# Optimization experiments

Hardware: AMD Instinct MI355X
Metric: run time of the kernel (lower is better)

Reference implementation:

```python
import jax, jax.numpy as jnp
import numpy as np

N = 100000   # nodes
E = 1600000  # directed edges
HID = 64


def gat_conv(x, src, dst, W, a_src, a_dst, b, heads, out_ch):
    """PyG-style GATConv (add_self_loops=True, negative_slope=0.2, concat)."""
    n = x.shape[0]
    h = (x @ W).reshape(n, heads, out_ch)              # [N,H,C]
    loop = jnp.arange(n, dtype=src.dtype)
    s = jnp.concatenate([src, loop])                   # self loops appended
    d = jnp.concatenate([dst, loop])
    alpha_src = jnp.sum(h * a_src, axis=-1)            # [N,H]
    alpha_dst = jnp.sum(h * a_dst, axis=-1)            # [N,H]
    alpha = jax.nn.leaky_relu(alpha_src[s] + alpha_dst[d], 0.2)  # [E+N,H]
    # segment softmax over incoming edges of each destination node
    amax = jax.ops.segment_max(alpha, d, num_segments=n)
    alpha = jnp.exp(alpha - amax[d])
    asum = jax.ops.segment_sum(alpha, d, num_segments=n)
    alpha = alpha / (asum[d] + 1e-16)
    msg = h[s] * alpha[:, :, None]                     # [E+N,H,C]
    out = jax.ops.segment_sum(msg, d, num_segments=n)  # [N,H,C]
    return out.reshape(n, heads * out_ch) + b


def setup_inputs() -> dict:
    key = jax.random.key(0)
    ks = jax.random.split(key, 22)
    rn = lambda k, shp, s=0.1: (jax.random.normal(k, shp, jnp.float32) * s)
    inp = {
        "x": jax.random.normal(ks[0], (N, 2), jnp.float32),
        "edge_index": jax.random.randint(ks[1], (2, E), 0, N, dtype=jnp.int32),
        "edge_attr": jax.random.normal(ks[2], (E, 2), jnp.float32),
        # node encoder
        "enc_W": rn(ks[3], (2, HID)), "enc_b": rn(ks[4], (HID,)),
        # gat1: heads=4, out=16
        "g1_W": rn(ks[5], (HID, HID)), "g1_as": rn(ks[6], (4, 16)),
        "g1_ad": rn(ks[7], (4, 16)), "g1_b": rn(ks[8], (HID,)),
        # gat2: heads=1, out=64
        "g2_W": rn(ks[9], (HID, HID)), "g2_as": rn(ks[10], (1, HID)),
        "g2_ad": rn(ks[11], (1, HID)), "g2_b": rn(ks[12], (HID,)),
        # node head
        "no_W1": rn(ks[13], (HID, HID)), "no_b1": rn(ks[14], (HID,)),
        "no_W2": rn(ks[15], (HID, 2)), "no_b2": rn(ks[16], (2,)),
        # edge head: in = 2*HID + 2 = 130
        "eo_W1": rn(ks[17], (2 * HID + 2, HID)), "eo_b1": rn(ks[18], (HID,)),
        "eo_W2": rn(ks[19], (HID, 1)), "eo_b2": rn(ks[20], (1,)),
    }
    return inp


def reference(x, edge_index, edge_attr, enc_W, enc_b,
              g1_W, g1_as, g1_ad, g1_b,
              g2_W, g2_as, g2_ad, g2_b,
              no_W1, no_b1, no_W2, no_b2,
              eo_W1, eo_b1, eo_W2, eo_b2):
    src, dst = edge_index[0], edge_index[1]
    h = x @ enc_W + enc_b                                    # node encoder (dropout = eval identity)
    h = jax.nn.elu(gat_conv(h, src, dst, g1_W, g1_as, g1_ad, g1_b, 4, 16))
    h = gat_conv(h, src, dst, g2_W, g2_as, g2_ad, g2_b, 1, HID)
    e_in = jnp.concatenate([h[src], h[dst], edge_attr], axis=-1)  # [E,130]
    node_pred = jnp.tanh(jax.nn.leaky_relu(h @ no_W1 + no_b1, 0.01) @ no_W2 + no_b2)
    edge_pred = jnp.tanh(jax.nn.leaky_relu(e_in @ eo_W1 + eo_b1, 0.01) @ eo_W2 + eo_b2)[:, 0]
    return edge_pred, node_pred
```

## Files before the change

### kernel.cpp

```cpp
#include <hip/hip_runtime.h>
#include <hip/hip_fp16.h>
#include <math.h>


typedef _Float16 half8_t __attribute__((ext_vector_type(8)));
typedef float floatx4 __attribute__((ext_vector_type(4)));

__global__ void k_scatter(const int* __restrict__ src, const int* __restrict__ dst,
                          int E, int NB, int cap, int* cursor,
                          unsigned int* __restrict__ ebuf,
                          const float* __restrict__ encW, const float* __restrict__ encb,
                          const float* __restrict__ g1W, float* __restrict__ Mc){
  __shared__ int hist[256];
  __shared__ int base[256];
  int t = threadIdx.x;
  if (blockIdx.x == 0 && t < 64){
    float m0 = 0.f, m1 = 0.f, cc = 0.f;
    for (int k = 0; k < 64; ++k){
      float g = g1W[k * 64 + t];
      m0 = fmaf(encW[k], g, m0);
      m1 = fmaf(encW[64 + k], g, m1);
      cc = fmaf(encb[k], g, cc);
    }
    Mc[t] = m0; Mc[64 + t] = m1; Mc[128 + t] = cc;
  }
  hist[t] = 0;
  __syncthreads();
  int cbase = blockIdx.x * 2048;
  int sv[8], bk[8], dl[8];
  #pragma unroll
  for (int i = 0; i < 8; ++i){
    int e = cbase + i * 256 + t;
    if (e < E){
      int d = dst[e];
      sv[i] = src[e]; bk[i] = d >> 9; dl[i] = d & 511;
      atomicAdd(&hist[bk[i]], 1);
    } else bk[i] = -1;
  }
  __syncthreads();
  int c = hist[t];
  base[t] = (t < NB && c > 0) ? (t * cap + atomicAdd(&cursor[t], c)) : 0;
  __syncthreads();
  hist[t] = 0;
  __syncthreads();
  #pragma unroll
  for (int i = 0; i < 8; ++i){
    if (bk[i] >= 0){
      int r = atomicAdd(&hist[bk[i]], 1);
      int p = base[bk[i]] + r;
      if (p < (bk[i] + 1) * cap)
        ebuf[p] = (unsigned)sv[i] | ((unsigned)dl[i] << 17);
    }
  }
}

__global__ void k_bucket_build(const int* __restrict__ cursor, int cap, int N,
                               unsigned int* ebuf, int* __restrict__ rstart,
                               int* __restrict__ rend){
  __shared__ unsigned int ent[12288];
  __shared__ int cnts[512];
  __shared__ int aux[512];
  int b = blockIdx.x, t = threadIdx.x;
  int base = b * cap;
  int cnt = cursor[b];
  if (cnt > cap) cnt = cap;
  for (int i = t; i < cnt; i += 512) ent[i] = ebuf[base + i];
  cnts[t] = 0;
  __syncthreads();
  for (int i = t; i < cnt; i += 512) atomicAdd(&cnts[ent[i] >> 17], 1);
  __syncthreads();
  int v = cnts[t];
  aux[t] = v;
  __syncthreads();
  for (int off = 1; off < 512; off <<= 1){
    int x = (t >= off) ? aux[t - off] : 0;
    __syncthreads();
    aux[t] += x;
    __syncthreads();
  }
  int incl = aux[t];
  int node = (b << 9) + t;
  if (node < N){ rstart[node] = base + incl - v; rend[node] = base + incl; }
  cnts[t] = incl - v;
  __syncthreads();
  for (int i = t; i < cnt; i += 512){
    unsigned int en = ent[i];
    int pos = atomicAdd(&cnts[en >> 17], 1);
    ebuf[base + pos] = en;
  }
}

template<int H>
__global__ void k_palpha(const int* __restrict__ cursor, int cap,
                         const unsigned int* __restrict__ ebuf,
                         const float* __restrict__ as, const float* __restrict__ ad,
                         float* __restrict__ palpha){
  int blk = blockIdx.x;
  int b = blk >> 2, part = blk & 3;
  int base = b * cap;
  int cnt = cursor[b];
  if (cnt > cap) cnt = cap;
  for (int i = part * 256 + threadIdx.x; i < cnt; i += 1024){
    unsigned int en = ebuf[base + i];
    int s = en & 0x1FFFFu;
    int d = (b << 9) + (en >> 17);
    if (H == 4){
      float4 sv = ((const float4*)as)[s];
      float4 dv = ((const float4*)ad)[d];
      float a0 = sv.x + dv.x, a1 = sv.y + dv.y, a2 = sv.z + dv.z, a3 = sv.w + dv.w;
      a0 = a0 > 0.f ? a0 : 0.2f * a0;
      a1 = a1 > 0.f ? a1 : 0.2f * a1;
      a2 = a2 > 0.f ? a2 : 0.2f * a2;
      a3 = a3 > 0.f ? a3 : 0.2f * a3;
      float4 pv = {__expf(a0), __expf(a1), __expf(a2), __expf(a3)};
      ((float4*)palpha)[base + i] = pv;
    } else {
      float a = as[s] + ad[d];
      a = a > 0.f ? a : 0.2f * a;
      palpha[base + i] = __expf(a);
    }
  }
}

__global__ void k_fuse1(const float* __restrict__ x, const float* __restrict__ Mc,
                        const float* __restrict__ a_s, const float* __restrict__ a_d,
                        __half* __restrict__ hw, float* __restrict__ alpha_s,
                        float* __restrict__ alpha_d, int n){
  int idx = blockIdx.x * blockDim.x + threadIdx.x;
  if (idx >= n * 64) return;
  int node = idx >> 6, j = idx & 63;
  float acc = fmaf(x[node * 2 + 0], Mc[j], fmaf(x[node * 2 + 1], Mc[64 + j], Mc[128 + j]));
  hw[idx] = __float2half(acc);
  float ps = acc * a_s[j];
  float pd = acc * a_d[j];
  #pragma unroll
  for (int off = 1; off < 16; off <<= 1){
    ps += __shfl_xor(ps, off);
    pd += __shfl_xor(pd, off);
  }
  if ((j & 15) == 0){
    int h = j >> 4;
    alpha_s[node * 4 + h] = ps;
    alpha_d[node * 4 + h] = pd;
  }
}

__global__ __launch_bounds__(256) void k_hw_mfma(
    const float* __restrict__ hin, const float* __restrict__ W,
    const float* __restrict__ a_s, const float* __restrict__ a_d,
    __half* __restrict__ hw, float* __restrict__ alpha_s,
    float* __restrict__ alpha_d, int n){
  __shared__ float redS[4][16];
  __shared__ float redD[4][16];
  int t = threadIdx.x;
  int lane = t & 63, wave = t >> 6;
  int l15 = lane & 15, quad = lane >> 4;
  int ch = wave * 16 + l15;
  half8_t b0, b1;
  #pragma unroll
  for (int j = 0; j < 8; ++j){
    b0[j] = (_Float16)W[(quad * 8 + j) * 64 + ch];
    b1[j] = (_Float16)W[(quad * 8 + j + 32) * 64 + ch];
  }
  float asv = a_s[ch], adv = a_d[ch];
  int base = blockIdx.x * 64;
  for (int it = 0; it < 4; ++it){
    int tb = base + it * 16;
    if (tb >= n) break;
    int arn = tb + l15; if (arn >= n) arn = n - 1;
    const float* arow = hin + (size_t)arn * 64 + quad * 8;
    half8_t a0, a1;
    #pragma unroll
    for (int j = 0; j < 8; ++j){
      a0[j] = (_Float16)arow[j];
      a1[j] = (_Float16)arow[j + 32];
    }
    floatx4 acc = {0.f, 0.f, 0.f, 0.f};
    acc = __builtin_amdgcn_mfma_f32_16x16x32_f16(a0, b0, acc, 0, 0, 0);
    acc = __builtin_amdgcn_mfma_f32_16x16x32_f16(a1, b1, acc, 0, 0, 0);
    float ps[4], pd[4];
    #pragma unroll
    for (int r = 0; r < 4; ++r){
      int node = tb + quad * 4 + r;
      if (node < n) hw[(size_t)node * 64 + ch] = __float2half(acc[r]);
      ps[r] = acc[r] * asv;
      pd[r] = acc[r] * adv;
      #pragma unroll
      for (int off = 1; off < 16; off <<= 1){
        ps[r] += __shfl_xor(ps[r], off);
        pd[r] += __shfl_xor(pd[r], off);
      }
    }
    if (l15 == 0){
      #pragma unroll
      for (int r = 0; r < 4; ++r){
        redS[wave][quad * 4 + r] = ps[r];
        redD[wave][quad * 4 + r] = pd[r];
      }
    }
    __syncthreads();
    if (t < 16 && tb + t < n){
      alpha_s[tb + t] = redS[0][t] + redS[1][t] + redS[2][t] + redS[3][t];
      alpha_d[tb + t] = redD[0][t] + redD[1][t] + redD[2][t] + redD[3][t];
    }
    __syncthreads();
  }
}

template<int H, bool ELU_ACT>
__global__ void k_agg(const __half* __restrict__ hw, const float* __restrict__ palpha,
                      const float* __restrict__ alpha_s, const float* __restrict__ alpha_d,
                      const int* __restrict__ rstart, const int* __restrict__ rend,
                      const unsigned int* __restrict__ ebuf,
                      const float* __restrict__ bias, float* __restrict__ hout, int n){
  int node = (blockIdx.x * blockDim.x + threadIdx.x) >> 6;
  int lane = threadIdx.x & 63;
  int g = lane >> 3, jj = lane & 7;
  if (node >= n) return;
  int hidx = (jj * H) >> 3;
  int start = rstart[node], end = rend[node];
  float acc[8] = {0.f,0.f,0.f,0.f,0.f,0.f,0.f,0.f};
  float psum = 0.f;
  if (g == 0){
    float a = alpha_s[node * H + hidx] + alpha_d[node * H + hidx];
    a = a > 0.f ? a : 0.2f * a;
    float p = __expf(a);
    psum = p;
    float4 rv = *(const float4*)(hw + (size_t)node * 64 + jj * 8);
    const __half2* hp = (const __half2*)&rv;
    #pragma unroll
    for (int k = 0; k < 4; ++k){
      float2 f = __half22float2(hp[k]);
      acc[2 * k] = p * f.x; acc[2 * k + 1] = p * f.y;
    }
  }
  int i = start + g;
  for (; i + 8 < end; i += 16){
    unsigned int e0 = ebuf[i], e1 = ebuf[i + 8];
    int s0 = e0 & 0x1FFFF, s1 = e1 & 0x1FFFF;
    float p0 = palpha[(size_t)i * H + hidx];
    float p1 = palpha[(size_t)(i + 8) * H + hidx];
    float4 r0 = *(const float4*)(hw + (size_t)s0 * 64 + jj * 8);
    float4 r1 = *(const float4*)(hw + (size_t)s1 * 64 + jj * 8);
    const __half2* h0 = (const __half2*)&r0;
    const __half2* h1 = (const __half2*)&r1;
    psum += p0 + p1;
    #pragma unroll
    for (int k = 0; k < 4; ++k){
      float2 f0 = __half22float2(h0[k]);
      float2 f1 = __half22float2(h1[k]);
      acc[2 * k]     = fmaf(p0, f0.x, fmaf(p1, f1.x, acc[2 * k]));
      acc[2 * k + 1] = fmaf(p0, f0.y, fmaf(p1, f1.y, acc[2 * k + 1]));
    }
  }
  if (i < end){
    unsigned int en = ebuf[i];
    int s = en & 0x1FFFF;
    float p = palpha[(size_t)i * H + hidx];
    float4 rv = *(const float4*)(hw + (size_t)s * 64 + jj * 8);
    const __half2* hp = (const __half2*)&rv;
    psum += p;
    #pragma unroll
    for (int k = 0; k < 4; ++k){
      float2 f = __half22float2(hp[k]);
      acc[2 * k]     = fmaf(p, f.x, acc[2 * k]);
      acc[2 * k + 1] = fmaf(p, f.y, acc[2 * k + 1]);
    }
  }
  #pragma unroll
  for (int off = 8; off < 64; off <<= 1){
    psum += __shfl_xor(psum, off);
    #pragma unroll
    for (int k = 0; k < 8; ++k) acc[k] += __shfl_xor(acc[k], off);
  }
  if (g == 0){
    float inv = 1.f / (psum + 1e-16f);
    float4 bv0 = ((const float4*)bias)[2 * jj];
    float4 bv1 = ((const float4*)bias)[2 * jj + 1];
    float o[8];
    o[0] = fmaf(acc[0], inv, bv0.x); o[1] = fmaf(acc[1], inv, bv0.y);
    o[2] = fmaf(acc[2], inv, bv0.z); o[3] = fmaf(acc[3], inv, bv0.w);
    o[4] = fmaf(acc[4], inv, bv1.x); o[5] = fmaf(acc[5], inv, bv1.y);
    o[6] = fmaf(acc[6], inv, bv1.z); o[7] = fmaf(acc[7], inv, bv1.w);
    if (ELU_ACT){
      #pragma unroll
      for (int k = 0; k < 8; ++k) o[k] = o[k] > 0.f ? o[k] : (__expf(o[k]) - 1.f);
    }
    float4 ov0 = {o[0], o[1], o[2], o[3]};
    float4 ov1 = {o[4], o[5], o[6], o[7]};
    float* dstp = hout + (size_t)node * 64 + jj * 8;
    *(float4*)dstp = ov0;
    *(float4*)(dstp + 4) = ov1;
  }
}

__global__ __launch_bounds__(256) void k_heads_mfma(
    const float* __restrict__ h, const float* __restrict__ eoW1,
    const float* __restrict__ noW1, const float* __restrict__ nob1,
    const float* __restrict__ noW2, const float* __restrict__ nob2,
    __half* __restrict__ P1, __half* __restrict__ P2,
    float* __restrict__ outN, int n){
  __shared__ float redP[4][16][2];
  int t = threadIdx.x;
  int lane = t & 63, wave = t >> 6;
  int l15 = lane & 15, quad = lane >> 4;
  int ch = wave * 16 + l15;
  half8_t bP1a, bP1b, bP2a, bP2b, bNa, bNb;
  #pragma unroll
  for (int j = 0; j < 8; ++j){
    int k0 = quad * 8 + j, k1 = k0 + 32;
    bP1a[j] = (_Float16)eoW1[k0 * 64 + ch];
    bP1b[j] = (_Float16)eoW1[k1 * 64 + ch];
    bP2a[j] = (_Float16)eoW1[(k0 + 64) * 64 + ch];
    bP2b[j] = (_Float16)eoW1[(k1 + 64) * 64 + ch];
    bNa[j]  = (_Float16)noW1[k0 * 64 + ch];
    bNb[j]  = (_Float16)noW1[k1 * 64 + ch];
  }
  float b1v = nob1[ch];
  float w20 = noW2[ch * 2 + 0], w21 = noW2[ch * 2 + 1];
  float b20 = nob2[0], b21 = nob2[1];
  int base = blockIdx.x * 64;
  for (int it = 0; it < 4; ++it){
    int tb = base + it * 16;
    if (tb >= n) break;
    int arn = tb + l15; if (arn >= n) arn = n - 1;
    const float* arow = h + (size_t)arn * 64 + quad * 8;
    half8_t a0, a1;
    #pragma unroll
    for (int j = 0; j < 8; ++j){
      a0[j] = (_Float16)arow[j];
      a1[j] = (_Float16)arow[j + 32];
    }
    floatx4 ac1 = {0.f,0.f,0.f,0.f}, ac2 = {0.f,0.f,0.f,0.f}, acN = {0.f,0.f,0.f,0.f};
    ac1 = __builtin_amdgcn_mfma_f32_16x16x32_f16(a0, bP1a, ac1, 0, 0, 0);
    ac1 = __builtin_amdgcn_mfma_f32_16x16x32_f16(a1, bP1b, ac1, 0, 0, 0);
    ac2 = __builtin_amdgcn_mfma_f32_16x16x32_f16(a0, bP2a, ac2, 0, 0, 0);
    ac2 = __builtin_amdgcn_mfma_f32_16x16x32_f16(a1, bP2b, ac2, 0, 0, 0);
    acN = __builtin_amdgcn_mfma_f32_16x16x32_f16(a0, bNa, acN, 0, 0, 0);
    acN = __builtin_amdgcn_mfma_f32_16x16x32_f16(a1, bNb, acN, 0, 0, 0);
    float p0[4], p1[4];
    #pragma unroll
    for (int r = 0; r < 4; ++r){
      int node = tb + quad * 4 + r;
      if (node < n){
        P1[(size_t)node * 64 + ch] = __float2half(ac1[r]);
        P2[(size_t)node * 64 + ch] = __float2half(ac2[r]);
      }
      float v = acN[r] + b1v;
      v = v > 0.f ? v : 0.01f * v;
      p0[r] = v * w20;
      p1[r] = v * w21;
      #pragma unroll
      for (int off = 1; off < 16; off <<= 1){
        p0[r] += __shfl_xor(p0[r], off);
        p1[r] += __shfl_xor(p1[r], off);
      }
    }
    if (l15 == 0){
      #pragma unroll
      for (int r = 0; r < 4; ++r){
        redP[wave][quad * 4 + r][0] = p0[r];
        redP[wave][quad * 4 + r][1] = p1[r];
      }
    }
    __syncthreads();
    if (t < 16 && tb + t < n){
      float s0 = redP[0][t][0] + redP[1][t][0] + redP[2][t][0] + redP[3][t][0];
      float s1 = redP[0][t][1] + redP[1][t][1] + redP[2][t][1] + redP[3][t][1];
      outN[(size_t)(tb + t) * 2 + 0] = tanhf(s0 + b20);
      outN[(size_t)(tb + t) * 2 + 1] = tanhf(s1 + b21);
    }
    __syncthreads();
  }
}

__global__ void k_edge_head(const __half* __restrict__ P1h, const __half* __restrict__ P2h,
                            const int* __restrict__ src, const int* __restrict__ dst,
                            const float* __restrict__ eattr, const float* __restrict__ eoW1,
                            const float* __restrict__ b1, const float* __restrict__ W2,
                            const float* __restrict__ b2, float* __restrict__ out, int E){
  int lane = threadIdx.x & 63;
  int jj = lane & 7, q = lane >> 3;
  int wid = (blockIdx.x * blockDim.x + threadIdx.x) >> 6;
  int nw = (gridDim.x * blockDim.x) >> 6;

  const float4* rAq = (const float4*)(eoW1 + 8192);
  const float4* rBq = (const float4*)(eoW1 + 8256);
  const float4* b1q = (const float4*)b1;
  const float4* w2q = (const float4*)W2;
  float4 tA0 = rAq[2 * jj], tA1 = rAq[2 * jj + 1];
  float4 tB0 = rBq[2 * jj], tB1 = rBq[2 * jj + 1];
  float4 tb0 = b1q[2 * jj], tb1 = b1q[2 * jj + 1];
  float4 tw0 = w2q[2 * jj], tw1 = w2q[2 * jj + 1];
  float ra[8] = {tA0.x, tA0.y, tA0.z, tA0.w, tA1.x, tA1.y, tA1.z, tA1.w};
  float rb[8] = {tB0.x, tB0.y, tB0.z, tB0.w, tB1.x, tB1.y, tB1.z, tB1.w};
  float bb[8] = {tb0.x, tb0.y, tb0.z, tb0.w, tb1.x, tb1.y, tb1.z, tb1.w};
  float w2[8] = {tw0.x, tw0.y, tw0.z, tw0.w, tw1.x, tw1.y, tw1.z, tw1.w};
  float b2v = b2[0];

  const float4* P1q = (const float4*)P1h;
  const float4* P2q = (const float4*)P2h;
  const float2* eav = (const float2*)eattr;

  int groups = (E + 15) >> 4;
  for (int g = wid; g < groups; g += nw){
    int e0 = g * 16 + q, e1 = e0 + 8;
    bool act0 = (e0 < E), act1 = (e1 < E);
    float p0 = 0.f, p1 = 0.f;
    if (act0){
      int s = src[e0], d = dst[e0];
      float2 ea = eav[e0];
      float4 g1 = P1q[(size_t)s * 8 + jj];
      float4 g2 = P2q[(size_t)d * 8 + jj];
      const __half2* h1 = (const __half2*)&g1;
      const __half2* h2 = (const __half2*)&g2;
      #pragma unroll
      for (int k = 0; k < 4; ++k){
        float2 u = __half22float2(h1[k]);
        float2 w = __half22float2(h2[k]);
        float ta = u.x + w.x + bb[2 * k];
        float tb = u.y + w.y + bb[2 * k + 1];
        ta = fmaf(ea.x, ra[2 * k], fmaf(ea.y, rb[2 * k], ta));
        tb = fmaf(ea.x, ra[2 * k + 1], fmaf(ea.y, rb[2 * k + 1], tb));
        ta = ta > 0.f ? ta : 0.01f * ta;
        tb = tb > 0.f ? tb : 0.01f * tb;
        p0 = fmaf(ta, w2[2 * k], fmaf(tb, w2[2 * k + 1], p0));
      }
    }
    if (act1){
      int s = src[e1], d = dst[e1];
      float2 ea = eav[e1];
      float4 g1 = P1q[(size_t)s * 8 + jj];
      float4 g2 = P2q[(size_t)d * 8 + jj];
      const __half2* h1 = (const __half2*)&g1;
      const __half2* h2 = (const __half2*)&g2;
      #pragma unroll
      for (int k = 0; k < 4; ++k){
        float2 u = __half22float2(h1[k]);
        float2 w = __half22float2(h2[k]);
        float ta = u.x + w.x + bb[2 * k];
        float tb = u.y + w.y + bb[2 * k + 1];
        ta = fmaf(ea.x, ra[2 * k], fmaf(ea.y, rb[2 * k], ta));
        tb = fmaf(ea.x, ra[2 * k + 1], fmaf(ea.y, rb[2 * k + 1], tb));
        ta = ta > 0.f ? ta : 0.01f * ta;
        tb = tb > 0.f ? tb : 0.01f * tb;
        p1 = fmaf(ta, w2[2 * k], fmaf(tb, w2[2 * k + 1], p1));
      }
    }
    #pragma unroll
    for (int off = 1; off < 8; off <<= 1){
      p0 += __shfl_xor(p0, off);
      p1 += __shfl_xor(p1, off);
    }
    if (jj == 0){
      if (act0) out[e0] = tanhf(p0 + b2v);
      if (act1) out[e1] = tanhf(p1 + b2v);
    }
  }
}

extern "C" void kernel_launch(void* const* d_in, const int* in_sizes, int n_in,
                              void* d_out, int out_size, void* d_ws, size_t ws_size,
                              hipStream_t stream){
  const float* x    = (const float*)d_in[0];
  const int*   eidx = (const int*)  d_in[1];
  const float* ea   = (const float*)d_in[2];
  const float* encW = (const float*)d_in[3];
  const float* encb = (const float*)d_in[4];
  const float* g1W  = (const float*)d_in[5];
  const float* g1as = (const float*)d_in[6];
  const float* g1ad = (const float*)d_in[7];
  const float* g1b  = (const float*)d_in[8];
  const float* g2W  = (const float*)d_in[9];
  const float* g2as = (const float*)d_in[10];
  const float* g2ad = (const float*)d_in[11];
  const float* g2b  = (const float*)d_in[12];
  const float* noW1 = (const float*)d_in[13];
  const float* nob1 = (const float*)d_in[14];
  const float* noW2 = (const float*)d_in[15];
  const float* nob2 = (const float*)d_in[16];
  const float* eoW1 = (const float*)d_in[17];
  const float* eob1 = (const float*)d_in[18];
  const float* eoW2 = (const float*)d_in[19];
  const float* eob2 = (const float*)d_in[20];

  const int N = in_sizes[0] / 2;
  const int E = in_sizes[1] / 2;
  const int* src = eidx;
  const int* dst = eidx + E;

  const int NB = (N + 511) >> 9;
  int avg = (E + NB - 1) / NB;
  int cap = avg + avg / 4 + 64;
  if (cap > 12288) cap = 12288;

  char* ws = (char*)d_ws;
  size_t off = 0;
  auto alloc = [&](size_t bytes) -> void* {
    void* p = ws + off;
    off = (off + bytes + 255) & ~(size_t)255;
    return p;
  };
  float*  bufA  = (float*) alloc((size_t)N * 64 * 4);
  __half* bufH  = (__half*)alloc((size_t)N * 64 * 2);
  __half* P1h   = (__half*)alloc((size_t)N * 64 * 2);
  __half* P2h   = (__half*)alloc((size_t)N * 64 * 2);
  float*  as    = (float*) alloc((size_t)N * 4 * 4);
  float*  ad    = (float*) alloc((size_t)N * 4 * 4);
  int* rstart   = (int*)   alloc((size_t)N * 4);
  int* rend     = (int*)   alloc((size_t)N * 4);
  unsigned int* ebuf = (unsigned int*)alloc((size_t)NB * cap * 4);
  float* palphaB = (float*)alloc((size_t)NB * cap * 16);
  int* cursor   = (int*)   alloc((size_t)NB * 4);
  float* Mc     = (float*) alloc(192 * 4);

  hipMemsetAsync(cursor, 0, (size_t)NB * 4, stream);
  k_scatter<<<(E + 2047) / 2048, 256, 0, stream>>>(src, dst, E, NB, cap, cursor, ebuf,
                                                   encW, encb, g1W, Mc);
  k_fuse1<<<(N * 64 + 255) / 256, 256, 0, stream>>>(x, Mc, g1as, g1ad, bufH, as, ad, N);
  k_bucket_build<<<NB, 512, 0, stream>>>(cursor, cap, N, ebuf, rstart, rend);
  k_palpha<4><<<NB * 4, 256, 0, stream>>>(cursor, cap, ebuf, as, ad, palphaB);
  k_agg<4, true><<<(N + 3) / 4, 256, 0, stream>>>(bufH, palphaB, as, ad,
                                                  rstart, rend, ebuf, g1b, bufA, N);
  k_hw_mfma<<<(N + 63) / 64, 256, 0, stream>>>(bufA, g2W, g2as, g2ad, bufH, as, ad, N);
  k_palpha<1><<<NB * 4, 256, 0, stream>>>(cursor, cap, ebuf, as, ad, palphaB);
  k_agg<1, false><<<(N + 3) / 4, 256, 0, stream>>>(bufH, palphaB, as, ad,
                                                   rstart, rend, ebuf, g2b, bufA, N);
  float* out = (float*)d_out;
  k_heads_mfma<<<(N + 63) / 64, 256, 0, stream>>>(bufA, eoW1, noW1, nob1, noW2, nob2,
                                                  P1h, P2h, out + E, N);
  k_edge_head<<<2048, 256, 0, stream>>>(P1h, P2h, src, dst, ea,
                                        eoW1, eob1, eoW2, eob2, out, E);
}
```

Before: 384.5 us.

## Shrink destination buckets to 128 nodes and store intermediate features in fp16

Destination buckets for the CSR build go from 512 nodes to 128. That gives about 782 buckets with smaller shared-memory footprints, so k_bucket_build can run with more blocks, less LDS per block and 256 threads. The scatter kernel's histogram loops now iterate over NB, since NB exceeds the thread count. Separately, the aggregation output is stored as fp16 rather than fp32, and the downstream MFMA kernels read it with vector half8 loads, halving that traffic and dropping the per-element conversions. Risks: many more global cursor atomics in the scatter step, a small cap of 2700 that could overflow buckets, and lower intermediate precision.

```diff
diff --git a/kernel.cpp b/kernel.cpp
--- a/kernel.cpp
+++ b/kernel.cpp
@@ -11,8 +11,8 @@
                           unsigned int* __restrict__ ebuf,
                           const float* __restrict__ encW, const float* __restrict__ encb,
                           const float* __restrict__ g1W, float* __restrict__ Mc){
-  __shared__ int hist[256];
-  __shared__ int base[256];
+  __shared__ int hist[800];
+  __shared__ int base[800];
   int t = threadIdx.x;
   if (blockIdx.x == 0 && t < 64){
     float m0 = 0.f, m1 = 0.f, cc = 0.f;
@@ -24,7 +24,7 @@
     }
     Mc[t] = m0; Mc[64 + t] = m1; Mc[128 + t] = cc;
   }
-  hist[t] = 0;
+  for (int i = t; i < NB; i += 256) hist[i] = 0;
   __syncthreads();
   int cbase = blockIdx.x * 2048;
   int sv[8], bk[8], dl[8];
@@ -33,15 +33,16 @@
     int e = cbase + i * 256 + t;
     if (e < E){
       int d = dst[e];
-      sv[i] = src[e]; bk[i] = d >> 9; dl[i] = d & 511;
+      sv[i] = src[e]; bk[i] = d >> 7; dl[i] = d & 127;
       atomicAdd(&hist[bk[i]], 1);
     } else bk[i] = -1;
   }
   __syncthreads();
-  int c = hist[t];
-  base[t] = (t < NB && c > 0) ? (t * cap + atomicAdd(&cursor[t], c)) : 0;
-  __syncthreads();
-  hist[t] = 0;
+  for (int i = t; i < NB; i += 256){
+    int c = hist[i];
+    base[i] = (c > 0) ? (i * cap + atomicAdd(&cursor[i], c)) : 0;
+    hist[i] = 0;
+  }
   __syncthreads();
   #pragma unroll
   for (int i = 0; i < 8; ++i){
@@ -57,33 +58,36 @@
 __global__ void k_bucket_build(const int* __restrict__ cursor, int cap, int N,
                                unsigned int* ebuf, int* __restrict__ rstart,
                                int* __restrict__ rend){
-  __shared__ unsigned int ent[12288];
-  __shared__ int cnts[512];
-  __shared__ int aux[512];
+  __shared__ unsigned int ent[2700];
+  __shared__ int cnts[128];
+  __shared__ int aux[128];
   int b = blockIdx.x, t = threadIdx.x;
   int base = b * cap;
   int cnt = cursor[b];
   if (cnt > cap) cnt = cap;
-  for (int i = t; i < cnt; i += 512) ent[i] = ebuf[base + i];
-  cnts[t] = 0;
-  __syncthreads();
-  for (int i = t; i < cnt; i += 512) atomicAdd(&cnts[ent[i] >> 17], 1);
-  __syncthreads();
-  int v = cnts[t];
-  aux[t] = v;
-  __syncthreads();
-  for (int off = 1; off < 512; off <<= 1){
-    int x = (t >= off) ? aux[t - off] : 0;
+  for (int i = t; i < cnt; i += 256) ent[i] = ebuf[base + i];
+  if (t < 128) cnts[t] = 0;
+  __syncthreads();
+  for (int i = t; i < cnt; i += 256) atomicAdd(&cnts[ent[i] >> 17], 1);
+  __syncthreads();
+  int v = 0;
+  if (t < 128){ v = cnts[t]; aux[t] = v; }
+  __syncthreads();
+  for (int off = 1; off < 128; off <<= 1){
+    int x = 0;
+    if (t < 128 && t >= off) x = aux[t - off];
     __syncthreads();
-    aux[t] += x;
+    if (t < 128) aux[t] += x;
     __syncthreads();
   }
-  int incl = aux[t];
-  int node = (b << 9) + t;
-  if (node < N){ rstart[node] = base + incl - v; rend[node] = base + incl; }
-  cnts[t] = incl - v;
-  __syncthreads();
-  for (int i = t; i < cnt; i += 512){
+  if (t < 128){
+    int incl = aux[t];
+    int node = (b << 7) + t;
+    if (node < N){ rstart[node] = base + incl - v; rend[node] = base + incl; }
+    cnts[t] = incl - v;
+  }
+  __syncthreads();
+  for (int i = t; i < cnt; i += 256){
     unsigned int en = ent[i];
     int pos = atomicAdd(&cnts[en >> 17], 1);
     ebuf[base + pos] = en;
@@ -103,7 +107,7 @@
   for (int i = part * 256 + threadIdx.x; i < cnt; i += 1024){
     unsigned int en = ebuf[base + i];
     int s = en & 0x1FFFFu;
-    int d = (b << 9) + (en >> 17);
+    int d = (b << 7) + (en >> 17);
     if (H == 4){
       float4 sv = ((const float4*)as)[s];
       float4 dv = ((const float4*)ad)[d];
@@ -146,7 +150,7 @@
 }
 
 __global__ __launch_bounds__(256) void k_hw_mfma(
-    const float* __restrict__ hin, const float* __restrict__ W,
+    const __half* __restrict__ hin, const float* __restrict__ W,
     const float* __restrict__ a_s, const float* __restrict__ a_d,
     __half* __restrict__ hw, float* __restrict__ alpha_s,
     float* __restrict__ alpha_d, int n){
@@ -168,13 +172,9 @@
     int tb = base + it * 16;
     if (tb >= n) break;
     int arn = tb + l15; if (arn >= n) arn = n - 1;
-    const float* arow = hin + (size_t)arn * 64 + quad * 8;
-    half8_t a0, a1;
-    #pragma unroll
-    for (int j = 0; j < 8; ++j){
-      a0[j] = (_Float16)arow[j];
-      a1[j] = (_Float16)arow[j + 32];
-    }
+    const __half* arow = hin + (size_t)arn * 64 + quad * 8;
+    half8_t a0 = *(const half8_t*)arow;
+    half8_t a1 = *(const half8_t*)(arow + 32);
     floatx4 acc = {0.f, 0.f, 0.f, 0.f};
     acc = __builtin_amdgcn_mfma_f32_16x16x32_f16(a0, b0, acc, 0, 0, 0);
     acc = __builtin_amdgcn_mfma_f32_16x16x32_f16(a1, b1, acc, 0, 0, 0);
@@ -212,7 +212,7 @@
                       const float* __restrict__ alpha_s, const float* __restrict__ alpha_d,
                       const int* __restrict__ rstart, const int* __restrict__ rend,
                       const unsigned int* __restrict__ ebuf,
-                      const float* __restrict__ bias, float* __restrict__ hout, int n){
+                      const float* __restrict__ bias, __half* __restrict__ hout, int n){
   int node = (blockIdx.x * blockDim.x + threadIdx.x) >> 6;
   int lane = threadIdx.x & 63;
   int g = lane >> 3, jj = lane & 7;
@@ -286,16 +286,15 @@
       #pragma unroll
       for (int k = 0; k < 8; ++k) o[k] = o[k] > 0.f ? o[k] : (__expf(o[k]) - 1.f);
     }
-    float4 ov0 = {o[0], o[1], o[2], o[3]};
-    float4 ov1 = {o[4], o[5], o[6], o[7]};
-    float* dstp = hout + (size_t)node * 64 + jj * 8;
-    *(float4*)dstp = ov0;
-    *(float4*)(dstp + 4) = ov1;
+    half8_t hv;
+    #pragma unroll
+    for (int k = 0; k < 8; ++k) hv[k] = (_Float16)o[k];
+    *(half8_t*)(hout + (size_t)node * 64 + jj * 8) = hv;
   }
 }
 
 __global__ __launch_bounds__(256) void k_heads_mfma(
-    const float* __restrict__ h, const float* __restrict__ eoW1,
+    const __half* __restrict__ h, const float* __restrict__ eoW1,
     const float* __restrict__ noW1, const float* __restrict__ nob1,
     const float* __restrict__ noW2, const float* __restrict__ nob2,
     __half* __restrict__ P1, __half* __restrict__ P2,
@@ -324,13 +323,9 @@
     int tb = base + it * 16;
     if (tb >= n) break;
     int arn = tb + l15; if (arn >= n) arn = n - 1;
-    const float* arow = h + (size_t)arn * 64 + quad * 8;
-    half8_t a0, a1;
-    #pragma unroll
-    for (int j = 0; j < 8; ++j){
-      a0[j] = (_Float16)arow[j];
-      a1[j] = (_Float16)arow[j + 32];
-    }
+    const __half* arow = h + (size_t)arn * 64 + quad * 8;
+    half8_t a0 = *(const half8_t*)arow;
+    half8_t a1 = *(const half8_t*)(arow + 32);
     floatx4 ac1 = {0.f,0.f,0.f,0.f}, ac2 = {0.f,0.f,0.f,0.f}, acN = {0.f,0.f,0.f,0.f};
     ac1 = __builtin_amdgcn_mfma_f32_16x16x32_f16(a0, bP1a, ac1, 0, 0, 0);
     ac1 = __builtin_amdgcn_mfma_f32_16x16x32_f16(a1, bP1b, ac1, 0, 0, 0);
@@ -489,10 +484,10 @@
   const int* src = eidx;
   const int* dst = eidx + E;
 
-  const int NB = (N + 511) >> 9;
+  const int NB = (N + 127) >> 7;
   int avg = (E + NB - 1) / NB;
   int cap = avg + avg / 4 + 64;
-  if (cap > 12288) cap = 12288;
+  if (cap > 2700) cap = 2700;
 
   char* ws = (char*)d_ws;
   size_t off = 0;
@@ -501,7 +496,7 @@
     off = (off + bytes + 255) & ~(size_t)255;
     return p;
   };
-  float*  bufA  = (float*) alloc((size_t)N * 64 * 4);
+  __half* bufA  = (__half*)alloc((size_t)N * 64 * 2);
   __half* bufH  = (__half*)alloc((size_t)N * 64 * 2);
   __half* P1h   = (__half*)alloc((size_t)N * 64 * 2);
   __half* P2h   = (__half*)alloc((size_t)N * 64 * 2);
@@ -518,7 +513,7 @@
   k_scatter<<<(E + 2047) / 2048, 256, 0, stream>>>(src, dst, E, NB, cap, cursor, ebuf,
                                                    encW, encb, g1W, Mc);
   k_fuse1<<<(N * 64 + 255) / 256, 256, 0, stream>>>(x, Mc, g1as, g1ad, bufH, as, ad, N);
-  k_bucket_build<<<NB, 512, 0, stream>>>(cursor, cap, N, ebuf, rstart, rend);
+  k_bucket_build<<<NB, 256, 0, stream>>>(cursor, cap, N, ebuf, rstart, rend);
   k_palpha<4><<<NB * 4, 256, 0, stream>>>(cursor, cap, ebuf, as, ad, palphaB);
   k_agg<4, true><<<(N + 3) / 4, 256, 0, stream>>>(bufH, palphaB, as, ad,
                                                   rstart, rend, ebuf, g1b, bufA, N);
```

After: 390.2 us. No clear change (+1.5%).
